# Performance work log

Measured on AMD Instinct MI355X. Metric: run time of the kernel, lower is better.

## Reference

```python
import jax, jax.numpy as jnp
import numpy as np

B, L1, L2, D, H, V, C = 32, 512, 16, 300, 300, 50000, 3


def setup_inputs() -> dict:
    key = jax.random.key(0)
    ks = jax.random.split(key, 20)
    s_emb = 1.0 / np.sqrt(D)
    s_h = 1.0 / np.sqrt(H)
    inp = {
        "context_ids": jax.random.randint(ks[0], (B, L1), 0, V),
        "aspect_ids": jax.random.randint(ks[1], (B, L2), 0, V),
        "context_masks": jnp.ones((B, L1), dtype=bool),
        "aspect_masks": jnp.ones((B, L2), dtype=bool),
        # frozen pretrained embedding table
        "emb": jax.random.normal(ks[2], (V, D), jnp.float32) * 0.1,
        # Attention module (no biases)
        "Wc": jax.random.normal(ks[3], (D, D), jnp.float32) * s_emb,
        "Wa": jax.random.normal(ks[4], (D, D), jnp.float32) * s_emb,
        "Vatt": jax.random.normal(ks[5], (1, D), jnp.float32) * s_emb,
        # self.W / self.V linears
        "Wlin": jax.random.normal(ks[6], (D, D), jnp.float32) * s_emb,
        "blin": jnp.zeros((D,), jnp.float32),
        "Vw": jax.random.normal(ks[7], (1, D), jnp.float32) * s_emb,
        "bVw": jnp.zeros((1,), jnp.float32),
        # bidirectional GRU, PyTorch layout: weight_ih (3H, D), weight_hh (3H, H)
        "wih_f": jax.random.normal(ks[8], (3 * H, D), jnp.float32) * s_h,
        "whh_f": jax.random.normal(ks[9], (3 * H, H), jnp.float32) * s_h,
        "bih_f": jnp.zeros((3 * H,), jnp.float32),
        "bhh_f": jnp.zeros((3 * H,), jnp.float32),
        "wih_b": jax.random.normal(ks[10], (3 * H, D), jnp.float32) * s_h,
        "whh_b": jax.random.normal(ks[11], (3 * H, H), jnp.float32) * s_h,
        "bih_b": jnp.zeros((3 * H,), jnp.float32),
        "bhh_b": jnp.zeros((3 * H,), jnp.float32),
        # output projection over concat(fwd, bwd) hidden
        "outW": jax.random.normal(ks[12], (C, 2 * H), jnp.float32) * (1.0 / np.sqrt(2 * H)),
        "outb": jnp.zeros((C,), jnp.float32),
    }
    return inp


def _gru_dir(x, wih, whh, bih, bhh, reverse):
    # x: (B, T, D) -> (B, T, H). PyTorch gate order: r, z, n.
    xg = jnp.einsum('btd,gd->btg', x, wih) + bih          # (B, T, 3H)
    xg = jnp.swapaxes(xg, 0, 1)                            # (T, B, 3H)

    def step(h, xg_t):
        rx, zx, nx = jnp.split(xg_t, 3, axis=-1)
        hg = h @ whh.T + bhh
        rh, zh, nh = jnp.split(hg, 3, axis=-1)
        r = jax.nn.sigmoid(rx + rh)
        z = jax.nn.sigmoid(zx + zh)
        n = jnp.tanh(nx + r * nh)
        h_new = (1.0 - z) * n + z * h
        return h_new, h_new

    h0 = jnp.zeros((x.shape[0], whh.shape[1]), x.dtype)
    _, hs = jax.lax.scan(step, h0, xg, reverse=reverse)
    return jnp.swapaxes(hs, 0, 1)                          # (B, T, H)


def reference(context_ids, aspect_ids, context_masks, aspect_masks, emb,
              Wc, Wa, Vatt, Wlin, blin, Vw, bVw,
              wih_f, whh_f, bih_f, bhh_f, wih_b, whh_b, bih_b, bhh_b,
              outW, outb):
    context = emb[context_ids]                             # (B, L1, D)
    aspect = emb[aspect_ids]                               # (B, L2, D)

    # additive (Bahdanau) attention: broadcast tanh score over (L1, L2)
    c = jnp.einsum('bld,ed->ble', context, Wc)             # (B, L1, D)
    a = jnp.einsum('bmd,ed->bme', aspect, Wa)              # (B, L2, D)
    s = jnp.tanh(c[:, :, None, :] + a[:, None, :, :])      # (B, L1, L2, D)
    scores = jnp.einsum('blmd,d->blm', s, Vatt[0])         # (B, L1, L2)
    alpha = jax.nn.softmax(scores, axis=-1)                # softmax over L2
    context_ = jnp.einsum('blm,bmd->bld', alpha, aspect)   # (B, L1, D)

    aaaa = jnp.tanh(jnp.einsum('bld,ed->ble', context, Wlin) + blin + context_)
    beta = jax.nn.softmax(jnp.einsum('bld,od->blo', aaaa, Vw) + bVw, axis=1)  # (B, L1, 1)

    h_f = _gru_dir(context, wih_f, whh_f, bih_f, bhh_f, reverse=False)
    h_b = _gru_dir(context, wih_b, whh_b, bih_b, bhh_b, reverse=True)
    senti_seq = jnp.concatenate([h_f, h_b], axis=-1)       # (B, L1, 2H)

    senti = jnp.einsum('bl,blh->bh', beta[..., 0], senti_seq)  # (B, 2H)
    logit = senti @ outW.T + outb                          # (B, C)
    return logit
```

## Files before the change

### kernel.cpp

```cpp
#include <hip/hip_runtime.h>

#define B_  32
#define L1_ 512
#define L2_ 16
#define D_  300
#define H_  300

__device__ __forceinline__ float sigmoid_fast(float x) {
    return 1.0f / (1.0f + __expf(-x));
}
__device__ __forceinline__ float tanh_fast(float x) {
    x = fminf(fmaxf(x, -15.0f), 15.0f);
    float e = __expf(2.0f * x);
    return (e - 1.0f) / (e + 1.0f);
}
__device__ __forceinline__ float sigmoid_acc(float x) {
    return 1.0f / (1.0f + expf(-x));
}
__device__ __forceinline__ float wred_sum(float v) {
    #pragma unroll
    for (int off = 32; off > 0; off >>= 1) v += __shfl_xor(v, off);
    return v;
}
__device__ __forceinline__ float wred_max(float v) {
    #pragma unroll
    for (int off = 32; off > 0; off >>= 1) v = fmaxf(v, __shfl_xor(v, off));
    return v;
}

__device__ __forceinline__ void store_pkt(long long* p, long long v) {
    asm volatile("global_store_dwordx2 %0, %1, off sc0 sc1" :: "v"(p), "v"(v) : "memory");
}
__device__ __forceinline__ long long load_pkt(const long long* p) {
    long long v;
    asm volatile("global_load_dwordx2 %0, %1, off sc0 sc1\n\t"
                 "s_waitcnt vmcnt(0)"
                 : "=v"(v) : "v"(p) : "memory");
    return v;
}
__device__ __forceinline__ void load_pkt2(const long long* p1, const long long* p2,
                                          long long& v1, long long& v2) {
    asm volatile("global_load_dwordx2 %0, %2, off sc0 sc1\n\t"
                 "global_load_dwordx2 %1, %3, off sc0 sc1\n\t"
                 "s_waitcnt vmcnt(0)"
                 : "=&v"(v1), "=v"(v2) : "v"(p1), "v"(p2) : "memory");
}

__global__ __launch_bounds__(256) void gather_kernel(const float* __restrict__ emb,
                                                     const int* __restrict__ ids,
                                                     float* __restrict__ out, int total) {
    for (int i = blockIdx.x * 256 + threadIdx.x; i < total; i += gridDim.x * 256) {
        int row = i / 75, c = i % 75;
        int id = ids[row];
        reinterpret_cast<float4*>(out)[i] =
            reinterpret_cast<const float4*>(emb + (size_t)id * 300)[c];
    }
}

#define TM 128
#define TN 64
#define TK 16
__device__ __forceinline__ int bcol(int c) { return c + ((c >> 5) << 2); }
__global__ __launch_bounds__(256) void gemm_nt(const float* __restrict__ A,
                                               const float* __restrict__ W,
                                               const float* __restrict__ bias,
                                               float* __restrict__ C,
                                               int M, int N, int K) {
    __shared__ __align__(16) float As[TK][TM + 4];
    __shared__ __align__(16) float Bs[TK][76];
    const int tid = threadIdx.x;
    const int m0 = blockIdx.x * TM;
    const int n0 = blockIdx.y * TN;
    const int tx = tid & 15;
    const int ty = tid >> 4;
    const int lr = tid >> 2;
    const int lk = (tid & 3) << 2;

    float acc[8][4];
    #pragma unroll
    for (int i = 0; i < 8; ++i)
        #pragma unroll
        for (int j = 0; j < 4; ++j) acc[i][j] = 0.f;

    for (int k0 = 0; k0 < K; k0 += TK) {
        const bool kok = (k0 + lk + 3) < K;
        #pragma unroll
        for (int h = 0; h < 2; ++h) {
            float4 v = make_float4(0.f, 0.f, 0.f, 0.f);
            int m = m0 + lr + 64 * h;
            if (kok) v = *reinterpret_cast<const float4*>(&A[(size_t)m * K + k0 + lk]);
            As[lk + 0][lr + 64 * h] = v.x;
            As[lk + 1][lr + 64 * h] = v.y;
            As[lk + 2][lr + 64 * h] = v.z;
            As[lk + 3][lr + 64 * h] = v.w;
        }
        {
            float4 v = make_float4(0.f, 0.f, 0.f, 0.f);
            int n = n0 + lr;
            if (kok && n < N) v = *reinterpret_cast<const float4*>(&W[(size_t)n * K + k0 + lk]);
            const int lrp = bcol(lr);
            Bs[lk + 0][lrp] = v.x;
            Bs[lk + 1][lrp] = v.y;
            Bs[lk + 2][lrp] = v.z;
            Bs[lk + 3][lrp] = v.w;
        }
        __syncthreads();
        #pragma unroll
        for (int k = 0; k < TK; ++k) {
            float4 a0 = *reinterpret_cast<const float4*>(&As[k][ty * 8]);
            float4 a1 = *reinterpret_cast<const float4*>(&As[k][ty * 8 + 4]);
            float4 bv = *reinterpret_cast<const float4*>(&Bs[k][bcol(tx * 4)]);
            float av[8] = {a0.x, a0.y, a0.z, a0.w, a1.x, a1.y, a1.z, a1.w};
            float bb[4] = {bv.x, bv.y, bv.z, bv.w};
            #pragma unroll
            for (int i = 0; i < 8; ++i)
                #pragma unroll
                for (int j = 0; j < 4; ++j) acc[i][j] += av[i] * bb[j];
        }
        __syncthreads();
    }
    #pragma unroll
    for (int i = 0; i < 8; ++i) {
        int m = m0 + ty * 8 + i;
        #pragma unroll
        for (int j = 0; j < 4; ++j) {
            int n = n0 + tx * 4 + j;
            if (n < N) C[(size_t)m * N + n] = acc[i][j] + (bias ? bias[n] : 0.f);
        }
    }
}

__global__ __launch_bounds__(256) void attn_kernel(const float* __restrict__ c_proj,
                                                   const float* __restrict__ a_proj,
                                                   const float* __restrict__ asp_emb,
                                                   const float* __restrict__ lin,
                                                   const float* __restrict__ Vatt,
                                                   const float* __restrict__ Vw,
                                                   const float* __restrict__ bVw,
                                                   float* __restrict__ blogit) {
    const int b = blockIdx.y;
    const int chunk = blockIdx.x;
    __shared__ float sA[16 * 300];
    __shared__ float sE[16 * 300];
    __shared__ float sV[300];
    __shared__ float sW[300];
    const int tid = threadIdx.x;
    for (int i = tid; i < 16 * 300; i += 256) {
        sA[i] = a_proj[b * 4800 + i];
        sE[i] = asp_emb[b * 4800 + i];
    }
    for (int i = tid; i < 300; i += 256) {
        sV[i] = Vatt[i];
        sW[i] = Vw[i];
    }
    __syncthreads();
    const int wave = tid >> 6, lane = tid & 63;
    const float bvw = bVw[0];
    for (int li = 0; li < 4; ++li) {
        const int l = chunk * 16 + wave * 4 + li;
        const float* crow = c_proj + (size_t)(b * L1_ + l) * 300;
        float cr[5];
        #pragma unroll
        for (int i = 0; i < 5; ++i) {
            int d = lane + 64 * i;
            cr[i] = (d < 300) ? crow[d] : 0.f;
        }
        float sc[16];
        #pragma unroll
        for (int m = 0; m < 16; ++m) {
            float s = 0.f;
            #pragma unroll
            for (int i = 0; i < 5; ++i) {
                int d = lane + 64 * i;
                if (d < 300) s += tanh_fast(cr[i] + sA[m * 300 + d]) * sV[d];
            }
            s = wred_sum(s);
            sc[m] = s;
        }
        float mx = sc[0];
        #pragma unroll
        for (int m = 1; m < 16; ++m) mx = fmaxf(mx, sc[m]);
        float den = 0.f;
        #pragma unroll
        for (int m = 0; m < 16; ++m) {
            sc[m] = __expf(sc[m] - mx);
            den += sc[m];
        }
        const float inv = 1.f / den;
        const float* lrow = lin + (size_t)(b * L1_ + l) * 300;
        float acc = 0.f;
        #pragma unroll
        for (int i = 0; i < 5; ++i) {
            int d = lane + 64 * i;
            if (d < 300) {
                float cd = 0.f;
                #pragma unroll
                for (int m = 0; m < 16; ++m) cd += sc[m] * sE[m * 300 + d];
                acc += tanh_fast(lrow[d] + cd * inv) * sW[d];
            }
        }
        acc = wred_sum(acc);
        if (lane == 0) blogit[b * L1_ + l] = acc + bvw;
    }
}

__global__ __launch_bounds__(256) void beta_softmax_kernel(const float* __restrict__ x,
                                                           float* __restrict__ y) {
    const int b = blockIdx.x, tid = threadIdx.x;
    __shared__ float red[4];
    const int wave = tid >> 6, lane = tid & 63;
    float v0 = x[b * 512 + tid];
    float v1 = x[b * 512 + 256 + tid];
    float m = wred_max(fmaxf(v0, v1));
    if (lane == 0) red[wave] = m;
    __syncthreads();
    m = fmaxf(fmaxf(red[0], red[1]), fmaxf(red[2], red[3]));
    float e0 = __expf(v0 - m), e1 = __expf(v1 - m);
    float s = wred_sum(e0 + e1);
    __syncthreads();
    if (lane == 0) red[wave] = s;
    __syncthreads();
    s = red[0] + red[1] + red[2] + red[3];
    const float inv = 1.f / s;
    y[b * 512 + tid] = e0 * inv;
    y[b * 512 + 256 + tid] = e1 * inv;
}

__global__ __launch_bounds__(256, 1) void gru8_kernel(const float* __restrict__ xg_f,
                                                      const float* __restrict__ xg_b,
                                                      const float* __restrict__ whh_f,
                                                      const float* __restrict__ whh_b,
                                                      const float* __restrict__ bhh_f,
                                                      const float* __restrict__ bhh_b,
                                                      const float* __restrict__ beta,
                                                      long long* __restrict__ slot,
                                                      float* __restrict__ senti) {
    const int s = blockIdx.x;
    const int b = blockIdx.y;
    const int rev = blockIdx.z;
    const int g = rev * 32 + b;
    const float* xg  = rev ? xg_b : xg_f;
    const float* whh = rev ? whh_b : whh_f;
    const float* bhh = rev ? bhh_b : bhh_f;

    const int tid = threadIdx.x;
    const int e0 = s * 75;
    const bool act = tid < 225;
    const int gate = tid / 75;
    const int idx = tid % 75;

    __shared__ __align__(16) float hs[304];
    __shared__ float gg[3][80];

    float4 w4[75];
    float bh = 0.f;
    if (act) {
        const int row = gate * 300 + e0 + idx;
        bh = bhh[row];
        const float4* wp = reinterpret_cast<const float4*>(whh + (size_t)row * 300);
        #pragma unroll
        for (int j = 0; j < 75; ++j) w4[j] = wp[j];
    } else {
        #pragma unroll
        for (int j = 0; j < 75; ++j) w4[j] = make_float4(0.f, 0.f, 0.f, 0.f);
    }
    #pragma unroll
    for (int j = 0; j < 75; ++j)
        asm volatile("" : "+v"(w4[j].x), "+v"(w4[j].y), "+v"(w4[j].z), "+v"(w4[j].w));
    asm volatile("" : "+v"(bh));

    int fsl1 = 0, fli1 = 0, fsl2 = 0, fli2 = 0;
    bool has2 = false;
    if (tid >= 128) {
        const int i1 = tid - 128;
        fsl1 = i1 / 75; if (fsl1 >= s) ++fsl1;
        fli1 = i1 % 75;
        const int i2 = i1 + 128;
        if (i2 < 225) {
            has2 = true;
            fsl2 = i2 / 75; if (fsl2 >= s) ++fsl2;
            fli2 = i2 % 75;
        } else {
            fsl2 = fsl1; fli2 = fli1;
        }
    }
    long long* wp0 = slot + ((size_t)g * 4 + s) * 80 + tid;
    const long long* rb1 = slot + ((size_t)g * 4 + fsl1) * 80 + fli1;
    const long long* rb2 = slot + ((size_t)g * 4 + fsl2) * 80 + fli2;

    for (int i = tid; i < 304; i += 256) hs[i] = 0.f;
    float sacc = 0.f;
    int gaveup = 0;
    __syncthreads();

    const float4* hs4 = reinterpret_cast<const float4*>(hs);
    for (int step = 0; step < 512; ++step) {
        const int t = rev ? (511 - step) : step;
        float xr = 0.f, xz = 0.f, xn = 0.f, bt = 0.f;
        if (tid < 75) {
            const float* xrow = xg + (size_t)(b * 512 + t) * 900;
            const int e = e0 + tid;
            xr = xrow[e];
            xz = xrow[300 + e];
            xn = xrow[600 + e];
            bt = beta[b * 512 + t];
        }
        float a0 = 0.f, a1 = 0.f, a2 = 0.f, a3 = 0.f;
        #pragma unroll
        for (int j = 0; j < 72; j += 4) {
            float4 hv;
            hv = hs4[j];
            a0 = fmaf(w4[j].x, hv.x, a0); a0 = fmaf(w4[j].y, hv.y, a0);
            a0 = fmaf(w4[j].z, hv.z, a0); a0 = fmaf(w4[j].w, hv.w, a0);
            hv = hs4[j + 1];
            a1 = fmaf(w4[j + 1].x, hv.x, a1); a1 = fmaf(w4[j + 1].y, hv.y, a1);
            a1 = fmaf(w4[j + 1].z, hv.z, a1); a1 = fmaf(w4[j + 1].w, hv.w, a1);
            hv = hs4[j + 2];
            a2 = fmaf(w4[j + 2].x, hv.x, a2); a2 = fmaf(w4[j + 2].y, hv.y, a2);
            a2 = fmaf(w4[j + 2].z, hv.z, a2); a2 = fmaf(w4[j + 2].w, hv.w, a2);
            hv = hs4[j + 3];
            a3 = fmaf(w4[j + 3].x, hv.x, a3); a3 = fmaf(w4[j + 3].y, hv.y, a3);
            a3 = fmaf(w4[j + 3].z, hv.z, a3); a3 = fmaf(w4[j + 3].w, hv.w, a3);
        }
        {
            float4 hv;
            hv = hs4[72];
            a0 = fmaf(w4[72].x, hv.x, a0); a0 = fmaf(w4[72].y, hv.y, a0);
            a0 = fmaf(w4[72].z, hv.z, a0); a0 = fmaf(w4[72].w, hv.w, a0);
            hv = hs4[73];
            a1 = fmaf(w4[73].x, hv.x, a1); a1 = fmaf(w4[73].y, hv.y, a1);
            a1 = fmaf(w4[73].z, hv.z, a1); a1 = fmaf(w4[73].w, hv.w, a1);
            hv = hs4[74];
            a2 = fmaf(w4[74].x, hv.x, a2); a2 = fmaf(w4[74].y, hv.y, a2);
            a2 = fmaf(w4[74].z, hv.z, a2); a2 = fmaf(w4[74].w, hv.w, a2);
        }
        const float acc = bh + ((a0 + a1) + (a2 + a3));
        if (act) gg[gate][idx] = acc;
        __syncthreads();
        if (step == 511) {
            if (tid < 75) {
                const float rr = sigmoid_acc(xr + gg[0][tid]);
                const float zz = sigmoid_acc(xz + gg[1][tid]);
                const float nn = tanhf(xn + rr * gg[2][tid]);
                const float hn = (1.f - zz) * nn + zz * hs[e0 + tid];
                sacc = fmaf(bt, hn, sacc);
            }
            break;
        }
        if (tid < 75) {
            const int e = e0 + tid;
            const float rr = sigmoid_acc(xr + gg[0][tid]);
            const float zz = sigmoid_acc(xz + gg[1][tid]);
            const float nn = tanhf(xn + rr * gg[2][tid]);
            const float hn = (1.f - zz) * nn + zz * hs[e];
            sacc = fmaf(bt, hn, sacc);
            hs[e] = hn;
            long long pkt = ((long long)(unsigned)step << 32) |
                            (unsigned)__float_as_int(hn);
            store_pkt(wp0 + (size_t)(step & 1) * 64 * 4 * 80, pkt);
        } else if (tid >= 128) {
            const size_t po = (size_t)(step & 1) * 64 * 4 * 80;
            const long long* p1 = rb1 + po;
            const long long* p2 = rb2 + po;
            long long v1 = 0, v2 = 0;
            if (!gaveup) {
                load_pkt2(p1, p2, v1, v2);
                int it = 0;
                while (((int)(v1 >> 32)) != step || ((int)(v2 >> 32)) != step) {
                    if (++it >= (1 << 16)) { gaveup = 1; break; }
                    __builtin_amdgcn_s_sleep(1);
                    load_pkt2(p1, p2, v1, v2);
                }
            } else {
                load_pkt2(p1, p2, v1, v2);
            }
            hs[fsl1 * 75 + fli1] = __int_as_float((int)(v1 & 0xffffffffLL));
            if (has2) hs[fsl2 * 75 + fli2] = __int_as_float((int)(v2 & 0xffffffffLL));
        }
        __syncthreads();
    }
    if (tid < 75) senti[b * 600 + rev * 300 + e0 + tid] = sacc;
}

__global__ __launch_bounds__(64) void logits_kernel(const float* __restrict__ senti,
                                                    const float* __restrict__ outW,
                                                    const float* __restrict__ outb,
                                                    float* __restrict__ out) {
    const int b = blockIdx.x, lane = threadIdx.x;
    for (int c = 0; c < 3; ++c) {
        float s = 0.f;
        for (int hh = lane; hh < 600; hh += 64) s += senti[b * 600 + hh] * outW[c * 600 + hh];
        s = wred_sum(s);
        if (lane == 0) out[b * 3 + c] = s + outb[c];
    }
}

extern "C" void kernel_launch(void* const* d_in, const int* in_sizes, int n_in,
                              void* d_out, int out_size, void* d_ws, size_t ws_size,
                              hipStream_t stream) {
    const int* ctx_ids = (const int*)d_in[0];
    const int* asp_ids = (const int*)d_in[1];
    const float* emb   = (const float*)d_in[4];
    const float* Wc    = (const float*)d_in[5];
    const float* Wa    = (const float*)d_in[6];
    const float* Vatt  = (const float*)d_in[7];
    const float* Wlin  = (const float*)d_in[8];
    const float* blin  = (const float*)d_in[9];
    const float* Vw    = (const float*)d_in[10];
    const float* bVw   = (const float*)d_in[11];
    const float* wih_f = (const float*)d_in[12];
    const float* whh_f = (const float*)d_in[13];
    const float* bih_f = (const float*)d_in[14];
    const float* bhh_f = (const float*)d_in[15];
    const float* wih_b = (const float*)d_in[16];
    const float* whh_b = (const float*)d_in[17];
    const float* bih_b = (const float*)d_in[18];
    const float* bhh_b = (const float*)d_in[19];
    const float* outW  = (const float*)d_in[20];
    const float* outb  = (const float*)d_in[21];
    float* ws = (float*)d_ws;

    size_t o = 0;
    float* ctx_emb = ws + o; o += (size_t)B_ * L1_ * D_;
    float* asp_emb = ws + o; o += (size_t)B_ * L2_ * D_;
    float* c_proj  = ws + o; o += (size_t)B_ * L1_ * D_;
    float* a_proj  = ws + o; o += (size_t)B_ * L2_ * D_;
    float* lin_buf = ws + o; o += (size_t)B_ * L1_ * D_;
    float* xg_f    = ws + o; o += (size_t)B_ * L1_ * 3 * H_;
    float* xg_b    = ws + o; o += (size_t)B_ * L1_ * 3 * H_;
    float* blogit  = ws + o; o += (size_t)B_ * L1_;
    float* beta    = ws + o; o += (size_t)B_ * L1_;
    float* senti   = ws + o; o += (size_t)B_ * 2 * H_;
    o = (o + 1) & ~(size_t)1;
    long long* slot = (long long*)(ws + o);
    const size_t slot_ll = (size_t)2 * 64 * 4 * 80;
    o += slot_ll * 2;

    hipMemsetAsync(slot, 0xFF, slot_ll * sizeof(long long), stream);

    dim3 blk(256);
    const int tot_ctx = B_ * L1_ * 75;
    const int tot_asp = B_ * L2_ * 75;
    gather_kernel<<<dim3((tot_ctx + 255) / 256), blk, 0, stream>>>(emb, ctx_ids, ctx_emb, tot_ctx);
    gather_kernel<<<dim3((tot_asp + 255) / 256), blk, 0, stream>>>(emb, asp_ids, asp_emb, tot_asp);

    gemm_nt<<<dim3(16384 / 128, 5), blk, 0, stream>>>(ctx_emb, Wc, nullptr, c_proj, 16384, 300, 300);
    gemm_nt<<<dim3(16384 / 128, 5), blk, 0, stream>>>(ctx_emb, Wlin, blin, lin_buf, 16384, 300, 300);
    gemm_nt<<<dim3(512 / 128, 5), blk, 0, stream>>>(asp_emb, Wa, nullptr, a_proj, 512, 300, 300);
    gemm_nt<<<dim3(16384 / 128, 15), blk, 0, stream>>>(ctx_emb, wih_f, bih_f, xg_f, 16384, 900, 300);
    gemm_nt<<<dim3(16384 / 128, 15), blk, 0, stream>>>(ctx_emb, wih_b, bih_b, xg_b, 16384, 900, 300);

    attn_kernel<<<dim3(32, 32), blk, 0, stream>>>(c_proj, a_proj, asp_emb, lin_buf, Vatt, Vw, bVw, blogit);
    beta_softmax_kernel<<<dim3(32), blk, 0, stream>>>(blogit, beta);
    gru8_kernel<<<dim3(4, 32, 2), blk, 0, stream>>>(xg_f, xg_b, whh_f, whh_b, bhh_f, bhh_b,
                                                    beta, slot, senti);
    logits_kernel<<<dim3(32), dim3(64), 0, stream>>>(senti, outW, outb, (float*)d_out);
}
```

Before: 2.464 ms.

## Interleave forward and backward GRU directions per block with 8-way hidden split

The GRU kernel changes from 4 blocks per (batch, direction) to 8 blocks per batch, each owning 38 hidden units of both directions. Within a step, one direction's matvec runs while the other direction's exchanged hidden state is polled from global slots, so cross-block communication latency is hidden behind compute. It also replaces __syncthreads with a lighter barrier, removes the polling sleep, and shortens the give-up limit. The cost is four barriers per step and more inter-block traffic, since each block now reads 262 remote values per direction.

```diff
diff --git a/kernel.cpp b/kernel.cpp
--- a/kernel.cpp
+++ b/kernel.cpp
@@ -31,19 +31,19 @@
 __device__ __forceinline__ void store_pkt(long long* p, long long v) {
     asm volatile("global_store_dwordx2 %0, %1, off sc0 sc1" :: "v"(p), "v"(v) : "memory");
 }
-__device__ __forceinline__ long long load_pkt(const long long* p) {
-    long long v;
-    asm volatile("global_load_dwordx2 %0, %1, off sc0 sc1\n\t"
-                 "s_waitcnt vmcnt(0)"
-                 : "=v"(v) : "v"(p) : "memory");
-    return v;
-}
 __device__ __forceinline__ void load_pkt2(const long long* p1, const long long* p2,
                                           long long& v1, long long& v2) {
     asm volatile("global_load_dwordx2 %0, %2, off sc0 sc1\n\t"
                  "global_load_dwordx2 %1, %3, off sc0 sc1\n\t"
                  "s_waitcnt vmcnt(0)"
-                 : "=&v"(v1), "=v"(v2) : "v"(p1), "v"(p2) : "memory");
+                 : "=&v"(v1), "=&v"(v2) : "v"(p1), "v"(p2) : "memory");
+}
+
+__device__ __forceinline__ void wg_barrier() {
+    __builtin_amdgcn_sched_barrier(0);
+    asm volatile("s_waitcnt lgkmcnt(0)" ::: "memory");
+    __builtin_amdgcn_s_barrier();
+    __builtin_amdgcn_sched_barrier(0);
 }
 
 __global__ __launch_bounds__(256) void gather_kernel(const float* __restrict__ emb,
@@ -226,7 +226,41 @@
     y[b * 512 + 256 + tid] = e1 * inv;
 }
 
-__global__ __launch_bounds__(256, 1) void gru8_kernel(const float* __restrict__ xg_f,
+__device__ __forceinline__ float matvec300(const float4* h4, const float4 (&w4)[75],
+                                           float bh) {
+    float a0 = 0.f, a1 = 0.f, a2 = 0.f, a3 = 0.f;
+    #pragma unroll
+    for (int j = 0; j < 72; j += 4) {
+        float4 hv;
+        hv = h4[j];
+        a0 = fmaf(w4[j].x, hv.x, a0); a0 = fmaf(w4[j].y, hv.y, a0);
+        a0 = fmaf(w4[j].z, hv.z, a0); a0 = fmaf(w4[j].w, hv.w, a0);
+        hv = h4[j + 1];
+        a1 = fmaf(w4[j + 1].x, hv.x, a1); a1 = fmaf(w4[j + 1].y, hv.y, a1);
+        a1 = fmaf(w4[j + 1].z, hv.z, a1); a1 = fmaf(w4[j + 1].w, hv.w, a1);
+        hv = h4[j + 2];
+        a2 = fmaf(w4[j + 2].x, hv.x, a2); a2 = fmaf(w4[j + 2].y, hv.y, a2);
+        a2 = fmaf(w4[j + 2].z, hv.z, a2); a2 = fmaf(w4[j + 2].w, hv.w, a2);
+        hv = h4[j + 3];
+        a3 = fmaf(w4[j + 3].x, hv.x, a3); a3 = fmaf(w4[j + 3].y, hv.y, a3);
+        a3 = fmaf(w4[j + 3].z, hv.z, a3); a3 = fmaf(w4[j + 3].w, hv.w, a3);
+    }
+    {
+        float4 hv;
+        hv = h4[72];
+        a0 = fmaf(w4[72].x, hv.x, a0); a0 = fmaf(w4[72].y, hv.y, a0);
+        a0 = fmaf(w4[72].z, hv.z, a0); a0 = fmaf(w4[72].w, hv.w, a0);
+        hv = h4[73];
+        a1 = fmaf(w4[73].x, hv.x, a1); a1 = fmaf(w4[73].y, hv.y, a1);
+        a1 = fmaf(w4[73].z, hv.z, a1); a1 = fmaf(w4[73].w, hv.w, a1);
+        hv = h4[74];
+        a2 = fmaf(w4[74].x, hv.x, a2); a2 = fmaf(w4[74].y, hv.y, a2);
+        a2 = fmaf(w4[74].z, hv.z, a2); a2 = fmaf(w4[74].w, hv.w, a2);
+    }
+    return bh + ((a0 + a1) + (a2 + a3));
+}
+
+__global__ __launch_bounds__(256, 1) void gru9_kernel(const float* __restrict__ xg_f,
                                                       const float* __restrict__ xg_b,
                                                       const float* __restrict__ whh_f,
                                                       const float* __restrict__ whh_b,
@@ -235,29 +269,29 @@
                                                       const float* __restrict__ beta,
                                                       long long* __restrict__ slot,
                                                       float* __restrict__ senti) {
-    const int s = blockIdx.x;
+    const int k = blockIdx.x;
     const int b = blockIdx.y;
-    const int rev = blockIdx.z;
-    const int g = rev * 32 + b;
-    const float* xg  = rev ? xg_b : xg_f;
-    const float* whh = rev ? whh_b : whh_f;
-    const float* bhh = rev ? bhh_b : bhh_f;
-
     const int tid = threadIdx.x;
-    const int e0 = s * 75;
-    const bool act = tid < 225;
-    const int gate = tid / 75;
-    const int idx = tid % 75;
-
-    __shared__ __align__(16) float hs[304];
-    __shared__ float gg[3][80];
+    const int e0 = k * 38;
+    const int own = (300 - e0 < 38) ? (300 - e0) : 38;
+    const int fcnt = 300 - own;
+
+    const bool isF = (tid < 114);
+    const bool isB = (tid >= 114) && (tid < 228);
+    int rgate = 0, ri = 0;
+    if (isF) { rgate = tid / 38; ri = tid % 38; }
+    else if (isB) { rgate = (tid - 114) / 38; ri = (tid - 114) % 38; }
+    const int re = e0 + ri;
+    const bool rowact = (isF || isB) && (re < 300);
+    const float* whhp = isB ? whh_b : whh_f;
+    const float* bhhp = isB ? bhh_b : bhh_f;
 
     float4 w4[75];
     float bh = 0.f;
-    if (act) {
-        const int row = gate * 300 + e0 + idx;
-        bh = bhh[row];
-        const float4* wp = reinterpret_cast<const float4*>(whh + (size_t)row * 300);
+    if (rowact) {
+        const int row = rgate * 300 + re;
+        bh = bhhp[row];
+        const float4* wp = reinterpret_cast<const float4*>(whhp + (size_t)row * 300);
         #pragma unroll
         for (int j = 0; j < 75; ++j) w4[j] = wp[j];
     } else {
@@ -269,117 +303,116 @@
         asm volatile("" : "+v"(w4[j].x), "+v"(w4[j].y), "+v"(w4[j].z), "+v"(w4[j].w));
     asm volatile("" : "+v"(bh));
 
-    int fsl1 = 0, fli1 = 0, fsl2 = 0, fli2 = 0;
-    bool has2 = false;
-    if (tid >= 128) {
-        const int i1 = tid - 128;
-        fsl1 = i1 / 75; if (fsl1 >= s) ++fsl1;
-        fli1 = i1 % 75;
-        const int i2 = i1 + 128;
-        if (i2 < 225) {
-            has2 = true;
-            fsl2 = i2 / 75; if (fsl2 >= s) ++fsl2;
-            fli2 = i2 % 75;
-        } else {
-            fsl2 = fsl1; fli2 = fli1;
-        }
-    }
-    long long* wp0 = slot + ((size_t)g * 4 + s) * 80 + tid;
-    const long long* rb1 = slot + ((size_t)g * 4 + fsl1) * 80 + fli1;
-    const long long* rb2 = slot + ((size_t)g * 4 + fsl2) * 80 + fli2;
-
-    for (int i = tid; i < 304; i += 256) hs[i] = 0.f;
-    float sacc = 0.f;
+    __shared__ __align__(16) float hs_f[304];
+    __shared__ __align__(16) float hs_b[304];
+    __shared__ float gg_f[3][40];
+    __shared__ float gg_b[3][40];
+    for (int i = tid; i < 304; i += 256) { hs_f[i] = 0.f; hs_b[i] = 0.f; }
+
+    const int ge = e0 + tid;
+    const bool gact = (tid < 38) && (ge < 300);
+
+    float sacc_f = 0.f, sacc_b = 0.f;
     int gaveup = 0;
     __syncthreads();
 
-    const float4* hs4 = reinterpret_cast<const float4*>(hs);
-    for (int step = 0; step < 512; ++step) {
-        const int t = rev ? (511 - step) : step;
-        float xr = 0.f, xz = 0.f, xn = 0.f, bt = 0.f;
-        if (tid < 75) {
-            const float* xrow = xg + (size_t)(b * 512 + t) * 900;
-            const int e = e0 + tid;
-            xr = xrow[e];
-            xz = xrow[300 + e];
-            xn = xrow[600 + e];
-            bt = beta[b * 512 + t];
-        }
-        float a0 = 0.f, a1 = 0.f, a2 = 0.f, a3 = 0.f;
-        #pragma unroll
-        for (int j = 0; j < 72; j += 4) {
-            float4 hv;
-            hv = hs4[j];
-            a0 = fmaf(w4[j].x, hv.x, a0); a0 = fmaf(w4[j].y, hv.y, a0);
-            a0 = fmaf(w4[j].z, hv.z, a0); a0 = fmaf(w4[j].w, hv.w, a0);
-            hv = hs4[j + 1];
-            a1 = fmaf(w4[j + 1].x, hv.x, a1); a1 = fmaf(w4[j + 1].y, hv.y, a1);
-            a1 = fmaf(w4[j + 1].z, hv.z, a1); a1 = fmaf(w4[j + 1].w, hv.w, a1);
-            hv = hs4[j + 2];
-            a2 = fmaf(w4[j + 2].x, hv.x, a2); a2 = fmaf(w4[j + 2].y, hv.y, a2);
-            a2 = fmaf(w4[j + 2].z, hv.z, a2); a2 = fmaf(w4[j + 2].w, hv.w, a2);
-            hv = hs4[j + 3];
-            a3 = fmaf(w4[j + 3].x, hv.x, a3); a3 = fmaf(w4[j + 3].y, hv.y, a3);
-            a3 = fmaf(w4[j + 3].z, hv.z, a3); a3 = fmaf(w4[j + 3].w, hv.w, a3);
-        }
-        {
-            float4 hv;
-            hv = hs4[72];
-            a0 = fmaf(w4[72].x, hv.x, a0); a0 = fmaf(w4[72].y, hv.y, a0);
-            a0 = fmaf(w4[72].z, hv.z, a0); a0 = fmaf(w4[72].w, hv.w, a0);
-            hv = hs4[73];
-            a1 = fmaf(w4[73].x, hv.x, a1); a1 = fmaf(w4[73].y, hv.y, a1);
-            a1 = fmaf(w4[73].z, hv.z, a1); a1 = fmaf(w4[73].w, hv.w, a1);
-            hv = hs4[74];
-            a2 = fmaf(w4[74].x, hv.x, a2); a2 = fmaf(w4[74].y, hv.y, a2);
-            a2 = fmaf(w4[74].z, hv.z, a2); a2 = fmaf(w4[74].w, hv.w, a2);
-        }
-        const float acc = bh + ((a0 + a1) + (a2 + a3));
-        if (act) gg[gate][idx] = acc;
-        __syncthreads();
-        if (step == 511) {
-            if (tid < 75) {
-                const float rr = sigmoid_acc(xr + gg[0][tid]);
-                const float zz = sigmoid_acc(xz + gg[1][tid]);
-                const float nn = tanhf(xn + rr * gg[2][tid]);
-                const float hn = (1.f - zz) * nn + zz * hs[e0 + tid];
-                sacc = fmaf(bt, hn, sacc);
-            }
-            break;
-        }
-        if (tid < 75) {
-            const int e = e0 + tid;
-            const float rr = sigmoid_acc(xr + gg[0][tid]);
-            const float zz = sigmoid_acc(xz + gg[1][tid]);
-            const float nn = tanhf(xn + rr * gg[2][tid]);
-            const float hn = (1.f - zz) * nn + zz * hs[e];
-            sacc = fmaf(bt, hn, sacc);
-            hs[e] = hn;
-            long long pkt = ((long long)(unsigned)step << 32) |
-                            (unsigned)__float_as_int(hn);
-            store_pkt(wp0 + (size_t)(step & 1) * 64 * 4 * 80, pkt);
-        } else if (tid >= 128) {
-            const size_t po = (size_t)(step & 1) * 64 * 4 * 80;
-            const long long* p1 = rb1 + po;
-            const long long* p2 = rb2 + po;
-            long long v1 = 0, v2 = 0;
+    const float4* hf4 = reinterpret_cast<const float4*>(hs_f);
+    const float4* hb4 = reinterpret_cast<const float4*>(hs_b);
+
+    for (int s = 0; s < 512; ++s) {
+        float xrf = 0.f, xzf = 0.f, xnf = 0.f, btf = 0.f;
+        float xrb = 0.f, xzb = 0.f, xnb = 0.f, btb = 0.f;
+        if (gact) {
+            const float* xf = xg_f + (size_t)(b * 512 + s) * 900;
+            xrf = xf[ge]; xzf = xf[300 + ge]; xnf = xf[600 + ge];
+            btf = beta[b * 512 + s];
+            const float* xb = xg_b + (size_t)(b * 512 + (511 - s)) * 900;
+            xrb = xb[ge]; xzb = xb[300 + ge]; xnb = xb[600 + ge];
+            btb = beta[b * 512 + (511 - s)];
+        }
+        if (isF) {
+            if (rowact) gg_f[rgate][ri] = matvec300(hf4, w4, bh);
+        } else if (s > 0) {
+            const int tag = s - 1;
+            const size_t base = ((size_t)((tag & 1) * 64 + b * 2 + 1)) * 304;
+            const int pid = tid - 114;
+            int f1 = pid;        if (f1 >= fcnt) f1 = fcnt - 1;
+            int f2 = pid + 142;  if (f2 >= fcnt) f2 = fcnt - 1;
+            const int ee1 = (f1 < e0) ? f1 : f1 + own;
+            const int ee2 = (f2 < e0) ? f2 : f2 + own;
+            const long long* p1 = slot + base + ee1;
+            const long long* p2 = slot + base + ee2;
+            long long v1, v2;
+            load_pkt2(p1, p2, v1, v2);
             if (!gaveup) {
-                load_pkt2(p1, p2, v1, v2);
                 int it = 0;
-                while (((int)(v1 >> 32)) != step || ((int)(v2 >> 32)) != step) {
-                    if (++it >= (1 << 16)) { gaveup = 1; break; }
-                    __builtin_amdgcn_s_sleep(1);
+                while (((int)(v1 >> 32)) != tag || ((int)(v2 >> 32)) != tag) {
+                    if (++it >= (1 << 14)) { gaveup = 1; break; }
                     load_pkt2(p1, p2, v1, v2);
                 }
-            } else {
-                load_pkt2(p1, p2, v1, v2);
-            }
-            hs[fsl1 * 75 + fli1] = __int_as_float((int)(v1 & 0xffffffffLL));
-            if (has2) hs[fsl2 * 75 + fli2] = __int_as_float((int)(v2 & 0xffffffffLL));
-        }
-        __syncthreads();
-    }
-    if (tid < 75) senti[b * 600 + rev * 300 + e0 + tid] = sacc;
+            }
+            hs_b[ee1] = __int_as_float((int)(v1 & 0xffffffffLL));
+            hs_b[ee2] = __int_as_float((int)(v2 & 0xffffffffLL));
+        }
+        wg_barrier();
+        if (gact) {
+            const float rr = sigmoid_acc(xrf + gg_f[0][tid]);
+            const float zz = sigmoid_acc(xzf + gg_f[1][tid]);
+            const float nn = tanhf(xnf + rr * gg_f[2][tid]);
+            const float hn = (1.f - zz) * nn + zz * hs_f[ge];
+            sacc_f = fmaf(btf, hn, sacc_f);
+            hs_f[ge] = hn;
+            if (s < 511) {
+                long long pkt = ((long long)(unsigned)s << 32) |
+                                (unsigned)__float_as_int(hn);
+                store_pkt(slot + ((size_t)((s & 1) * 64 + b * 2 + 0)) * 304 + ge, pkt);
+            }
+        }
+        wg_barrier();
+        if (isB) {
+            if (rowact) gg_b[rgate][ri] = matvec300(hb4, w4, bh);
+        } else if (s < 511) {
+            const int tag = s;
+            const size_t base = ((size_t)((tag & 1) * 64 + b * 2 + 0)) * 304;
+            const int pid = (tid < 114) ? tid : 114 + (tid - 228);
+            int f1 = pid;        if (f1 >= fcnt) f1 = fcnt - 1;
+            int f2 = pid + 142;  if (f2 >= fcnt) f2 = fcnt - 1;
+            const int ee1 = (f1 < e0) ? f1 : f1 + own;
+            const int ee2 = (f2 < e0) ? f2 : f2 + own;
+            const long long* p1 = slot + base + ee1;
+            const long long* p2 = slot + base + ee2;
+            long long v1, v2;
+            load_pkt2(p1, p2, v1, v2);
+            if (!gaveup) {
+                int it = 0;
+                while (((int)(v1 >> 32)) != tag || ((int)(v2 >> 32)) != tag) {
+                    if (++it >= (1 << 14)) { gaveup = 1; break; }
+                    load_pkt2(p1, p2, v1, v2);
+                }
+            }
+            hs_f[ee1] = __int_as_float((int)(v1 & 0xffffffffLL));
+            hs_f[ee2] = __int_as_float((int)(v2 & 0xffffffffLL));
+        }
+        wg_barrier();
+        if (gact) {
+            const float rr = sigmoid_acc(xrb + gg_b[0][tid]);
+            const float zz = sigmoid_acc(xzb + gg_b[1][tid]);
+            const float nn = tanhf(xnb + rr * gg_b[2][tid]);
+            const float hn = (1.f - zz) * nn + zz * hs_b[ge];
+            sacc_b = fmaf(btb, hn, sacc_b);
+            hs_b[ge] = hn;
+            if (s < 511) {
+                long long pkt = ((long long)(unsigned)s << 32) |
+                                (unsigned)__float_as_int(hn);
+                store_pkt(slot + ((size_t)((s & 1) * 64 + b * 2 + 1)) * 304 + ge, pkt);
+            }
+        }
+        wg_barrier();
+    }
+    if (gact) {
+        senti[b * 600 + ge] = sacc_f;
+        senti[b * 600 + 300 + ge] = sacc_b;
+    }
 }
 
 __global__ __launch_bounds__(64) void logits_kernel(const float* __restrict__ senti,
@@ -433,7 +466,7 @@
     float* senti   = ws + o; o += (size_t)B_ * 2 * H_;
     o = (o + 1) & ~(size_t)1;
     long long* slot = (long long*)(ws + o);
-    const size_t slot_ll = (size_t)2 * 64 * 4 * 80;
+    const size_t slot_ll = (size_t)2 * 32 * 2 * 304;
     o += slot_ll * 2;
 
     hipMemsetAsync(slot, 0xFF, slot_ll * sizeof(long long), stream);
@@ -452,7 +485,7 @@
 
     attn_kernel<<<dim3(32, 32), blk, 0, stream>>>(c_proj, a_proj, asp_emb, lin_buf, Vatt, Vw, bVw, blogit);
     beta_softmax_kernel<<<dim3(32), blk, 0, stream>>>(blogit, beta);
-    gru8_kernel<<<dim3(4, 32, 2), blk, 0, stream>>>(xg_f, xg_b, whh_f, whh_b, bhh_f, bhh_b,
-                                                    beta, slot, senti);
+    gru9_kernel<<<dim3(8, 32), blk, 0, stream>>>(xg_f, xg_b, whh_f, whh_b, bhh_f, bhh_b,
+                                                 beta, slot, senti);
     logits_kernel<<<dim3(32), dim3(64), 0, stream>>>(senti, outW, outb, (float*)d_out);
 }
```

Result: slower. 4.354 ms (+76.7%).
